# Optimization experiments

Measured on AMD Instinct MI355X. Metric: run time of the kernel, lower is better.

Reference implementation:

```python
import jax, jax.numpy as jnp
import numpy as np

C = 768       # hidden_dim
HEADS = 12    # num_heads
HDIM = C // HEADS  # 64


def _ln(x, w, eps=1e-5):
    # LayerNorm with weight, no bias (matches nn.LayerNorm(..., bias=False))
    mu = jnp.mean(x, axis=-1, keepdims=True)
    var = jnp.mean((x - mu) ** 2, axis=-1, keepdims=True)
    return (x - mu) * jax.lax.rsqrt(var + eps) * w


def _attn(q, k, v):
    # scaled dot product attention over the second-to-last axis
    scale = 1.0 / np.sqrt(q.shape[-1]).astype(np.float32)
    s = jnp.einsum('...qc,...kc->...qk', q, k) * scale
    return jnp.einsum('...qk,...kc->...qc', jax.nn.softmax(s, axis=-1), v)


def setup_inputs() -> dict:
    key = jax.random.key(0)
    ks = jax.random.split(key, 4)
    B, H, W = 4, 64, 64
    x = jax.random.normal(ks[0], (B, H, W, C), jnp.float32)
    Wqkv = jax.random.normal(ks[1], (C, 7 * C), jnp.float32) * 0.02
    bqkv = jnp.zeros((7 * C,), jnp.float32)
    Wout = jax.random.normal(ks[2], (C, C), jnp.float32) * 0.02
    bout = jnp.zeros((C,), jnp.float32)
    Wmlp = jax.random.normal(ks[3], (4 * C, C), jnp.float32) * 0.02
    bmlp = jnp.zeros((C,), jnp.float32)
    norm_w = jnp.ones((C,), jnp.float32)
    qnorm_w = jnp.ones((HDIM,), jnp.float32)
    knorm_w = jnp.ones((HDIM,), jnp.float32)
    gamma = jnp.full((C,), 1e-6, jnp.float32)
    return {"x": x, "norm_w": norm_w, "Wqkv": Wqkv, "bqkv": bqkv,
            "qnorm_w": qnorm_w, "knorm_w": knorm_w, "Wout": Wout,
            "bout": bout, "Wmlp": Wmlp, "bmlp": bmlp, "gamma": gamma}


def reference(x, norm_w, Wqkv, bqkv, qnorm_w, knorm_w, Wout, bout, Wmlp, bmlp, gamma):
    B, H, W, _ = x.shape
    xn = _ln(x, norm_w)
    proj = xn @ Wqkv + bqkv                       # (B,H,W,7C)
    q, k, v, ff = jnp.split(proj, [C, 2 * C, 3 * C], axis=-1)
    heads = lambda t: t.reshape(B, H, W, HEADS, HDIM)
    q, k, v = heads(q), heads(k), heads(v)        # (B,H,W,He,c)
    q = _ln(q, qnorm_w)
    k = _ln(k, knorm_w)

    # --- axis 1: 'b h w he c -> b h he w c', attend over w ---
    q, k, v = (t.transpose(0, 1, 3, 2, 4) for t in (q, k, v))  # (B,H,He,W,c)
    ax = _attn(q, k, v)                                         # (B,H,He,W,c)
    # out_permutation 'b w he h c -> b h w (he c)' applied POSITIONALLY ->
    # the first axis contribution lands spatially transposed (requires H==W)
    out = ax.transpose(0, 3, 1, 2, 4).reshape(B, W, H, C)

    # --- axis 2: 'b h he w c -> b w he h c' (positional), attend over h ---
    q, k, v = (t.transpose(0, 3, 2, 1, 4) for t in (q, k, v))  # (B,W,He,H,c)
    ax = _attn(q, k, v)                                         # (B,W,He,H,c)
    out = out + ax.transpose(0, 3, 1, 2, 4).reshape(B, H, W, C)

    y = out @ Wout + bout + (jax.nn.gelu(ff, approximate=False) @ Wmlp + bmlp)
    return x + gamma * y
```

## Files before the change

kernel.cpp:

```cpp
#include <hip/hip_runtime.h>

typedef unsigned short u16;
typedef unsigned int u32;
typedef unsigned char u8;
typedef long i64;
typedef float f4 __attribute__((ext_vector_type(4)));
typedef int i32x8 __attribute__((ext_vector_type(8)));

#define CDIM 768
#define NPROJ 5376
#define KFF 3840
#define NTOK 16384

__device__ __forceinline__ u8 f2fp8(float f) {
#if __has_builtin(__builtin_amdgcn_cvt_pk_fp8_f32)
    return (u8)(__builtin_amdgcn_cvt_pk_fp8_f32(f, f, 0, false) & 0xff);
#else
    u32 u = __float_as_uint(f);
    u32 s = (u >> 24) & 0x80u;
    float a = fabsf(f);
    a = fminf(a, 448.f);
    if (a < 0.015625f) return (u8)(s | (u32)(a * 512.f + 0.5f));
    u32 b = __float_as_uint(a);
    b += 0x0007FFFFu + ((b >> 20) & 1u);
    u32 e = b >> 23, m = (b >> 20) & 7u;
    u32 code = ((e - 120u) << 3) | m;
    if (code > 0x7Eu) code = 0x7Eu;
    return (u8)(s | code);
#endif
}
__device__ __forceinline__ u32 pk4_fp8(float a, float b, float c, float d) {
#if __has_builtin(__builtin_amdgcn_cvt_pk_fp8_f32)
    u32 lo = (u32)__builtin_amdgcn_cvt_pk_fp8_f32(a, b, 0, false);
    return (u32)__builtin_amdgcn_cvt_pk_fp8_f32(c, d, lo, true);
#else
    return (u32)f2fp8(a) | ((u32)f2fp8(b) << 8) | ((u32)f2fp8(c) << 16) | ((u32)f2fp8(d) << 24);
#endif
}
__device__ __forceinline__ float fp8_to_f32(u32 v) {
#if __has_builtin(__builtin_amdgcn_cvt_f32_fp8)
    return __builtin_amdgcn_cvt_f32_fp8((int)v, 0);
#else
    u32 s = v >> 7, e = (v >> 3) & 15u, m = v & 7u;
    float mag = e ? __uint_as_float(((e + 120u) << 23) | (m << 20))
                  : (float)m * 0.001953125f;
    return s ? -mag : mag;
#endif
}

__device__ __forceinline__ float wsum64(float v) {
#pragma unroll
    for (int m = 32; m > 0; m >>= 1) v += __shfl_xor(v, m, 64);
    return v;
}
__device__ __forceinline__ void gl_lds16(const u8* g, u8* l) {
    __builtin_amdgcn_global_load_lds((__attribute__((address_space(1))) u32*)g,
                                     (__attribute__((address_space(3))) u32*)l,
                                     16, 0, 0);
}

__global__ __launch_bounds__(256) void prep_fused(
    const float* __restrict__ Wqkv, u8* __restrict__ WqkvT,
    const float* __restrict__ Wout, const float* __restrict__ Wmlp,
    u8* __restrict__ BT2,
    const float* __restrict__ x, const float* __restrict__ normw,
    u8* __restrict__ xn) {
    __shared__ float t[32][33];
    const int bid = blockIdx.x;
    const int tid = threadIdx.x;
    if (bid < 6912) {
        const float* src; u8* dst; int R, Cc, dstride, doff, bx, by;
        if (bid < 4032) {
            src = Wqkv; dst = WqkvT; R = CDIM; Cc = NPROJ; dstride = CDIM; doff = 0;
            bx = bid % 168; by = bid / 168;
        } else if (bid < 4608) {
            const int b2 = bid - 4032;
            src = Wout; dst = BT2; R = CDIM; Cc = CDIM; dstride = KFF; doff = 0;
            bx = b2 % 24; by = b2 / 24;
        } else {
            const int b2 = bid - 4608;
            src = Wmlp; dst = BT2; R = 3072; Cc = CDIM; dstride = KFF; doff = 768;
            bx = b2 % 24; by = b2 / 24;
        }
        const int c0 = bx * 32, r0 = by * 32;
        const int tx = tid & 31, ty = tid >> 5;
#pragma unroll
        for (int i = 0; i < 32; i += 8) {
            int r = r0 + ty + i, c = c0 + tx;
            if (r < R && c < Cc) t[ty + i][tx] = src[(size_t)r * Cc + c];
        }
        __syncthreads();
#pragma unroll
        for (int i = 0; i < 32; i += 8) {
            int c = c0 + ty + i, r = r0 + tx;
            if (r < R && c < Cc) dst[(size_t)c * dstride + doff + r] = f2fp8(t[tx][ty + i]);
        }
    } else {
        const int row = (bid - 6912) * 4 + (tid >> 6);
        const int lane = tid & 63;
        const f4* xr = (const f4*)(x + (size_t)row * CDIM);
        const f4* wr = (const f4*)normw;
        f4 v[3];
        float s = 0.f, s2 = 0.f;
#pragma unroll
        for (int i = 0; i < 3; ++i) {
            v[i] = xr[lane + 64 * i];
#pragma unroll
            for (int j = 0; j < 4; ++j) { s += v[i][j]; s2 += v[i][j] * v[i][j]; }
        }
        s = wsum64(s); s2 = wsum64(s2);
        float mu = s * (1.f / 768.f);
        float var = s2 * (1.f / 768.f) - mu * mu;
        float rs = rsqrtf(var + 1e-5f);
        u32* xo = (u32*)(xn + (size_t)row * CDIM);
#pragma unroll
        for (int i = 0; i < 3; ++i) {
            f4 wv = wr[lane + 64 * i];
            xo[lane + 64 * i] = pk4_fp8((v[i][0] - mu) * rs * wv[0], (v[i][1] - mu) * rs * wv[1],
                                        (v[i][2] - mu) * rs * wv[2], (v[i][3] - mu) * rs * wv[3]);
        }
    }
}

template <int MODE>
__global__ __launch_bounds__(256) void gemm_bt(
    const u8* __restrict__ A, const u8* __restrict__ B, int M, int N, int K,
    const float* __restrict__ bias0, const float* __restrict__ bias1,
    const float* __restrict__ xres, const float* __restrict__ gamma,
    u8* __restrict__ oqkv, u8* __restrict__ off, float* __restrict__ ofin) {
    __shared__ __align__(16) u8 As[128 * 128];
    __shared__ __align__(16) u8 Bs[128 * 128];
    const int tid = threadIdx.x;
    const int wid = tid >> 6, lane = tid & 63;
    const int wm = wid >> 1, wn = wid & 1;
    const int quad = lane >> 4, l16 = lane & 15;
    const int m0 = blockIdx.y * 128, n0 = blockIdx.x * 128;

    f4 acc[4][4] = {};

    const int rl = lane >> 3;
    const int csw = ((lane & 7) ^ rl) * 16;
    const u8* aptr[4]; const u8* bptr[4];
    u8* alds[4]; u8* blds[4];
#pragma unroll
    for (int jj = 0; jj < 4; ++jj) {
        const int r0 = wid * 32 + jj * 8;
        aptr[jj] = A + (size_t)(m0 + r0 + rl) * K + csw;
        bptr[jj] = B + (size_t)(n0 + r0 + rl) * K + csw;
        alds[jj] = As + r0 * 128;
        blds[jj] = Bs + r0 * 128;
    }
    const int swl = l16 & 7;

    for (int kt = 0; kt < K; kt += 128) {
#pragma unroll
        for (int jj = 0; jj < 4; ++jj) {
            gl_lds16(aptr[jj] + kt, alds[jj]);
            gl_lds16(bptr[jj] + kt, blds[jj]);
        }
        __syncthreads();
        const int c0 = ((2 * quad) ^ swl) * 16;
        const int c1 = ((2 * quad + 1) ^ swl) * 16;
        i32x8 af[4], bfv[4];
#pragma unroll
        for (int mi = 0; mi < 4; ++mi) {
            const u8* base = As + (wm * 64 + mi * 16 + l16) * 128;
            uint4 lo = *(const uint4*)(base + c0);
            uint4 hi = *(const uint4*)(base + c1);
            af[mi][0] = lo.x; af[mi][1] = lo.y; af[mi][2] = lo.z; af[mi][3] = lo.w;
            af[mi][4] = hi.x; af[mi][5] = hi.y; af[mi][6] = hi.z; af[mi][7] = hi.w;
        }
#pragma unroll
        for (int ni = 0; ni < 4; ++ni) {
            const u8* base = Bs + (wn * 64 + ni * 16 + l16) * 128;
            uint4 lo = *(const uint4*)(base + c0);
            uint4 hi = *(const uint4*)(base + c1);
            bfv[ni][0] = lo.x; bfv[ni][1] = lo.y; bfv[ni][2] = lo.z; bfv[ni][3] = lo.w;
            bfv[ni][4] = hi.x; bfv[ni][5] = hi.y; bfv[ni][6] = hi.z; bfv[ni][7] = hi.w;
        }
#pragma unroll
        for (int mi = 0; mi < 4; ++mi)
#pragma unroll
            for (int ni = 0; ni < 4; ++ni)
                acc[mi][ni] = __builtin_amdgcn_mfma_scale_f32_16x16x128_f8f6f4(
                    af[mi], bfv[ni], acc[mi][ni], 0, 0, 0, 127, 0, 127);
        __syncthreads();
    }

#pragma unroll
    for (int mi = 0; mi < 4; ++mi) {
#pragma unroll
        for (int ni = 0; ni < 4; ++ni) {
            const int col = n0 + wn * 64 + ni * 16 + l16;
            const int rowb = m0 + wm * 64 + mi * 16 + quad * 4;
            if (MODE == 0) {
                const float bc = bias0[col];
#pragma unroll
                for (int r = 0; r < 4; ++r) {
                    float vv = acc[mi][ni][r] + bc;
                    const int m = rowb + r;
                    if (col < 2304) {
                        oqkv[(size_t)m * 2304 + col] = f2fp8(vv);
                    } else {
                        float u2 = vv * (-1.5957691216f) - 0.0713548162f * vv * vv * vv;
                        float g = vv / (1.f + __expf(u2));
                        off[(size_t)m * KFF + 768 + (col - 2304)] = f2fp8(g);
                    }
                }
            } else {
                const float bc = bias0[col] + bias1[col];
                const float gm = gamma[col];
#pragma unroll
                for (int r = 0; r < 4; ++r) {
                    const int m = rowb + r;
                    float vv = acc[mi][ni][r] + bc;
                    ofin[(size_t)m * CDIM + col] = xres[(size_t)m * CDIM + col] + gm * vv;
                }
            }
        }
    }
}

__global__ __launch_bounds__(256) void axial_attn_mfma(const u8* __restrict__ qkv,
                                                       const float* __restrict__ qnw,
                                                       const float* __restrict__ knw,
                                                       u8* __restrict__ A2) {
    __shared__ __align__(16) u8 Qs[64 * 72];
    __shared__ __align__(16) u8 Ks[64 * 72];
    __shared__ __align__(16) u8 Vt[64 * 72];
    __shared__ __align__(16) u8 Ps[64 * 72];

    const int bx = blockIdx.x;
    const int he = bx % 12;
    const int j = (bx / 12) & 63;
    const int b = bx / (12 * 64);
    const int tid = threadIdx.x;
    const int w = tid >> 6, lane = tid & 63;
    const int l16 = lane & 15, quad = lane >> 4;
    const int qb = w * 16;

    f4 acc_o[4] = {};

    const int sr = tid >> 2;
    const int sc = (tid & 3) * 16;
    const f4* qwv = (const f4*)(qnw + sc);
    const f4* kwv = (const f4*)(knw + sc);

    for (int phase = 0; phase < 2; ++phase) {
        const size_t tok = (phase == 0) ? (size_t)((b * 64 + j) * 64 + sr)
                                        : (size_t)((b * 64 + sr) * 64 + j);
        const u8* src = qkv + tok * 2304 + he * 64 + sc;
        {
            uint4 qv = *(const uint4*)(src);
            uint4 kv = *(const uint4*)(src + 768);
            const u32* qu = (const u32*)&qv;
            const u32* ku = (const u32*)&kv;
            float qf[16], kf[16];
#pragma unroll
            for (int jj = 0; jj < 4; ++jj)
#pragma unroll
                for (int bb = 0; bb < 4; ++bb) {
                    qf[jj * 4 + bb] = fp8_to_f32((qu[jj] >> (8 * bb)) & 0xffu);
                    kf[jj * 4 + bb] = fp8_to_f32((ku[jj] >> (8 * bb)) & 0xffu);
                }
            float s1q = 0.f, s2q = 0.f, s1k = 0.f, s2k = 0.f;
#pragma unroll
            for (int i = 0; i < 16; ++i) {
                s1q += qf[i]; s2q += qf[i] * qf[i];
                s1k += kf[i]; s2k += kf[i] * kf[i];
            }
            s1q += __shfl_xor(s1q, 1, 64); s1q += __shfl_xor(s1q, 2, 64);
            s2q += __shfl_xor(s2q, 1, 64); s2q += __shfl_xor(s2q, 2, 64);
            s1k += __shfl_xor(s1k, 1, 64); s1k += __shfl_xor(s1k, 2, 64);
            s2k += __shfl_xor(s2k, 1, 64); s2k += __shfl_xor(s2k, 2, 64);
            const float muq = s1q * (1.f / 64.f), muk = s1k * (1.f / 64.f);
            const float rsq = rsqrtf(s2q * (1.f / 64.f) - muq * muq + 1e-5f);
            const float rsk = rsqrtf(s2k * (1.f / 64.f) - muk * muk + 1e-5f);
            uint4 qo, ko;
            u32* qop = (u32*)&qo; u32* kop = (u32*)&ko;
#pragma unroll
            for (int jj = 0; jj < 4; ++jj) {
                const f4 wq = qwv[jj], wk = kwv[jj];
                qop[jj] = pk4_fp8((qf[jj * 4 + 0] - muq) * rsq * wq[0],
                                  (qf[jj * 4 + 1] - muq) * rsq * wq[1],
                                  (qf[jj * 4 + 2] - muq) * rsq * wq[2],
                                  (qf[jj * 4 + 3] - muq) * rsq * wq[3]);
                kop[jj] = pk4_fp8((kf[jj * 4 + 0] - muk) * rsk * wk[0],
                                  (kf[jj * 4 + 1] - muk) * rsk * wk[1],
                                  (kf[jj * 4 + 2] - muk) * rsk * wk[2],
                                  (kf[jj * 4 + 3] - muk) * rsk * wk[3]);
            }
            *(uint4*)(Qs + sr * 72 + sc) = qo;
            *(uint4*)(Ks + sr * 72 + sc) = ko;
        }
        {
            uint4 vv = *(const uint4*)(src + 1536);
            const u8* vb = (const u8*)&vv;
#pragma unroll
            for (int i = 0; i < 16; ++i) Vt[(sc + i) * 72 + sr] = vb[i];
        }
        __syncthreads();

        f4 st[4] = {};
#pragma unroll
        for (int kt = 0; kt < 2; ++kt) {
            const int boff = (kt * 4 + quad) * 8;
            const i64 bq = *(const i64*)(Qs + (qb + l16) * 72 + boff);
#pragma unroll
            for (int mt = 0; mt < 4; ++mt) {
                const i64 ak = *(const i64*)(Ks + (mt * 16 + l16) * 72 + boff);
                st[mt] = __builtin_amdgcn_mfma_f32_16x16x32_fp8_fp8(ak, bq, st[mt], 0, 0, 0);
            }
        }

        float sv[16];
        float mx = -1e30f;
#pragma unroll
        for (int mt = 0; mt < 4; ++mt)
#pragma unroll
            for (int r = 0; r < 4; ++r) {
                const float s = st[mt][r] * 0.125f;
                sv[mt * 4 + r] = s;
                mx = fmaxf(mx, s);
            }
        mx = fmaxf(mx, __shfl_xor(mx, 16, 64));
        mx = fmaxf(mx, __shfl_xor(mx, 32, 64));
        float sm = 0.f;
#pragma unroll
        for (int i = 0; i < 16; ++i) { sv[i] = __expf(sv[i] - mx); sm += sv[i]; }
        sm += __shfl_xor(sm, 16, 64);
        sm += __shfl_xor(sm, 32, 64);
        const float inv = 1.f / sm;

#pragma unroll
        for (int mt = 0; mt < 4; ++mt) {
            const int kbase = mt * 16 + quad * 4;
            *(u32*)(Ps + (qb + l16) * 72 + kbase) =
                pk4_fp8(sv[mt * 4] * inv, sv[mt * 4 + 1] * inv,
                        sv[mt * 4 + 2] * inv, sv[mt * 4 + 3] * inv);
        }
        __syncthreads();

#pragma unroll
        for (int kt = 0; kt < 2; ++kt) {
            const int boff = (kt * 4 + quad) * 8;
            const i64 ap = *(const i64*)(Ps + (qb + l16) * 72 + boff);
#pragma unroll
            for (int nt = 0; nt < 4; ++nt) {
                const i64 bv = *(const i64*)(Vt + (nt * 16 + l16) * 72 + boff);
                acc_o[nt] = __builtin_amdgcn_mfma_f32_16x16x32_fp8_fp8(ap, bv, acc_o[nt], 0, 0, 0);
            }
        }
        __syncthreads();
    }

#pragma unroll
    for (int nt = 0; nt < 4; ++nt)
#pragma unroll
        for (int r = 0; r < 4; ++r) {
            const int q = qb + quad * 4 + r;
            const int c = nt * 16 + l16;
            A2[((size_t)((b * 64 + q) * 64 + j)) * KFF + he * 64 + c] = f2fp8(acc_o[nt][r]);
        }
}

extern "C" void kernel_launch(void* const* d_in, const int* in_sizes, int n_in,
                              void* d_out, int out_size, void* d_ws, size_t ws_size,
                              hipStream_t stream) {
    const float* x = (const float*)d_in[0];
    const float* normw = (const float*)d_in[1];
    const float* Wqkv = (const float*)d_in[2];
    const float* bqkv = (const float*)d_in[3];
    const float* qnw = (const float*)d_in[4];
    const float* knw = (const float*)d_in[5];
    const float* Wout = (const float*)d_in[6];
    const float* bout = (const float*)d_in[7];
    const float* Wmlp = (const float*)d_in[8];
    const float* bmlp = (const float*)d_in[9];
    const float* gamma = (const float*)d_in[10];
    float* out = (float*)d_out;

    char* ws = (char*)d_ws;
    u8* xn = (u8*)ws;    ws += (size_t)NTOK * CDIM;
    u8* WqkvT = (u8*)ws; ws += (size_t)NPROJ * CDIM;
    u8* BT2 = (u8*)ws;   ws += (size_t)CDIM * KFF;
    u8* qkv = (u8*)ws;   ws += (size_t)NTOK * 2304;
    u8* A2 = (u8*)ws;    ws += (size_t)NTOK * KFF;

    prep_fused<<<11008, 256, 0, stream>>>(Wqkv, WqkvT, Wout, Wmlp, BT2, x, normw, xn);
    gemm_bt<0><<<dim3(NPROJ / 128, NTOK / 128), 256, 0, stream>>>(
        xn, WqkvT, NTOK, NPROJ, CDIM, bqkv, nullptr, nullptr, nullptr, qkv, A2, nullptr);
    axial_attn_mfma<<<3072, 256, 0, stream>>>(qkv, qnw, knw, A2);
    gemm_bt<1><<<dim3(CDIM / 128, NTOK / 128), 256, 0, stream>>>(
        A2, BT2, NTOK, CDIM, KFF, bout, bmlp, x, gamma, nullptr, nullptr, out);
}
```

Measured before the change: 367.9 us.

## Fuse per-head q/k LayerNorm into projection GEMM epilogue and remap block order

```diff
diff --git a/kernel.cpp b/kernel.cpp
--- a/kernel.cpp
+++ b/kernel.cpp
@@ -134,7 +134,12 @@
     const int wid = tid >> 6, lane = tid & 63;
     const int wm = wid >> 1, wn = wid & 1;
     const int quad = lane >> 4, l16 = lane & 15;
-    const int m0 = blockIdx.y * 128, n0 = blockIdx.x * 128;
+
+    const int nbx = (int)gridDim.x;
+    const int nwg = (int)(gridDim.x * gridDim.y);
+    int bid = (int)(blockIdx.y * gridDim.x + blockIdx.x);
+    bid = (bid & 7) * (nwg >> 3) + (bid >> 3);
+    const int m0 = (bid / nbx) * 128, n0 = (bid % nbx) * 128;
 
     f4 acc[4][4] = {};
 
@@ -187,34 +192,74 @@
         __syncthreads();
     }
 
+    const int cbase = n0 + wn * 64;
 #pragma unroll
     for (int mi = 0; mi < 4; ++mi) {
-#pragma unroll
-        for (int ni = 0; ni < 4; ++ni) {
-            const int col = n0 + wn * 64 + ni * 16 + l16;
-            const int rowb = m0 + wm * 64 + mi * 16 + quad * 4;
-            if (MODE == 0) {
-                const float bc = bias0[col];
+        const int rowb = m0 + wm * 64 + mi * 16 + quad * 4;
+        if (MODE == 0) {
+            if (cbase < 1536) {
+                const float* hw = (cbase < 768) ? xres : gamma;
+                float hwv[4], bc[4];
+#pragma unroll
+                for (int ni = 0; ni < 4; ++ni) {
+                    hwv[ni] = hw[ni * 16 + l16];
+                    bc[ni] = bias0[cbase + ni * 16 + l16];
+                }
 #pragma unroll
                 for (int r = 0; r < 4; ++r) {
-                    float vv = acc[mi][ni][r] + bc;
-                    const int m = rowb + r;
-                    if (col < 2304) {
-                        oqkv[(size_t)m * 2304 + col] = f2fp8(vv);
-                    } else {
+                    float v[4]; float s1 = 0.f, s2 = 0.f;
+#pragma unroll
+                    for (int ni = 0; ni < 4; ++ni) {
+                        v[ni] = acc[mi][ni][r] + bc[ni];
+                        s1 += v[ni]; s2 += v[ni] * v[ni];
+                    }
+#pragma unroll
+                    for (int mk = 1; mk <= 8; mk <<= 1) {
+                        s1 += __shfl_xor(s1, mk, 64);
+                        s2 += __shfl_xor(s2, mk, 64);
+                    }
+                    const float mu = s1 * (1.f / 64.f);
+                    const float rs = rsqrtf(s2 * (1.f / 64.f) - mu * mu + 1e-5f);
+                    const size_t m = (size_t)(rowb + r);
+#pragma unroll
+                    for (int ni = 0; ni < 4; ++ni)
+                        oqkv[m * 2304 + cbase + ni * 16 + l16] =
+                            f2fp8((v[ni] - mu) * rs * hwv[ni]);
+                }
+            } else if (cbase < 2304) {
+#pragma unroll
+                for (int ni = 0; ni < 4; ++ni) {
+                    const int col = cbase + ni * 16 + l16;
+                    const float bcv = bias0[col];
+#pragma unroll
+                    for (int r = 0; r < 4; ++r)
+                        oqkv[(size_t)(rowb + r) * 2304 + col] = f2fp8(acc[mi][ni][r] + bcv);
+                }
+            } else {
+#pragma unroll
+                for (int ni = 0; ni < 4; ++ni) {
+                    const int col = cbase + ni * 16 + l16;
+                    const float bcv = bias0[col];
+#pragma unroll
+                    for (int r = 0; r < 4; ++r) {
+                        float vv = acc[mi][ni][r] + bcv;
                         float u2 = vv * (-1.5957691216f) - 0.0713548162f * vv * vv * vv;
                         float g = vv / (1.f + __expf(u2));
-                        off[(size_t)m * KFF + 768 + (col - 2304)] = f2fp8(g);
+                        off[(size_t)(rowb + r) * KFF + 768 + (col - 2304)] = f2fp8(g);
                     }
                 }
-            } else {
-                const float bc = bias0[col] + bias1[col];
+            }
+        } else {
+#pragma unroll
+            for (int ni = 0; ni < 4; ++ni) {
+                const int col = cbase + ni * 16 + l16;
+                const float bcv = bias0[col] + bias1[col];
                 const float gm = gamma[col];
 #pragma unroll
                 for (int r = 0; r < 4; ++r) {
-                    const int m = rowb + r;
-                    float vv = acc[mi][ni][r] + bc;
-                    ofin[(size_t)m * CDIM + col] = xres[(size_t)m * CDIM + col] + gm * vv;
+                    const size_t m = (size_t)(rowb + r);
+                    float vv = acc[mi][ni][r] + bcv;
+                    ofin[m * CDIM + col] = xres[m * CDIM + col] + gm * vv;
                 }
             }
         }
@@ -222,15 +267,14 @@
 }
 
 __global__ __launch_bounds__(256) void axial_attn_mfma(const u8* __restrict__ qkv,
-                                                       const float* __restrict__ qnw,
-                                                       const float* __restrict__ knw,
                                                        u8* __restrict__ A2) {
     __shared__ __align__(16) u8 Qs[64 * 72];
     __shared__ __align__(16) u8 Ks[64 * 72];
     __shared__ __align__(16) u8 Vt[64 * 72];
     __shared__ __align__(16) u8 Ps[64 * 72];
 
-    const int bx = blockIdx.x;
+    int bx = (int)blockIdx.x;
+    bx = (bx & 7) * 384 + (bx >> 3);
     const int he = bx % 12;
     const int j = (bx / 12) & 63;
     const int b = bx / (12 * 64);
@@ -243,8 +287,6 @@
 
     const int sr = tid >> 2;
     const int sc = (tid & 3) * 16;
-    const f4* qwv = (const f4*)(qnw + sc);
-    const f4* kwv = (const f4*)(knw + sc);
 
     for (int phase = 0; phase < 2; ++phase) {
         const size_t tok = (phase == 0) ? (size_t)((b * 64 + j) * 64 + sr)
@@ -253,45 +295,8 @@
         {
             uint4 qv = *(const uint4*)(src);
             uint4 kv = *(const uint4*)(src + 768);
-            const u32* qu = (const u32*)&qv;
-            const u32* ku = (const u32*)&kv;
-            float qf[16], kf[16];
-#pragma unroll
-            for (int jj = 0; jj < 4; ++jj)
-#pragma unroll
-                for (int bb = 0; bb < 4; ++bb) {
-                    qf[jj * 4 + bb] = fp8_to_f32((qu[jj] >> (8 * bb)) & 0xffu);
-                    kf[jj * 4 + bb] = fp8_to_f32((ku[jj] >> (8 * bb)) & 0xffu);
-                }
-            float s1q = 0.f, s2q = 0.f, s1k = 0.f, s2k = 0.f;
-#pragma unroll
-            for (int i = 0; i < 16; ++i) {
-                s1q += qf[i]; s2q += qf[i] * qf[i];
-                s1k += kf[i]; s2k += kf[i] * kf[i];
-            }
-            s1q += __shfl_xor(s1q, 1, 64); s1q += __shfl_xor(s1q, 2, 64);
-            s2q += __shfl_xor(s2q, 1, 64); s2q += __shfl_xor(s2q, 2, 64);
-            s1k += __shfl_xor(s1k, 1, 64); s1k += __shfl_xor(s1k, 2, 64);
-            s2k += __shfl_xor(s2k, 1, 64); s2k += __shfl_xor(s2k, 2, 64);
-            const float muq = s1q * (1.f / 64.f), muk = s1k * (1.f / 64.f);
-            const float rsq = rsqrtf(s2q * (1.f / 64.f) - muq * muq + 1e-5f);
-            const float rsk = rsqrtf(s2k * (1.f / 64.f) - muk * muk + 1e-5f);
-            uint4 qo, ko;
-            u32* qop = (u32*)&qo; u32* kop = (u32*)&ko;
-#pragma unroll
-            for (int jj = 0; jj < 4; ++jj) {
-                const f4 wq = qwv[jj], wk = kwv[jj];
-                qop[jj] = pk4_fp8((qf[jj * 4 + 0] - muq) * rsq * wq[0],
-                                  (qf[jj * 4 + 1] - muq) * rsq * wq[1],
-                                  (qf[jj * 4 + 2] - muq) * rsq * wq[2],
-                                  (qf[jj * 4 + 3] - muq) * rsq * wq[3]);
-                kop[jj] = pk4_fp8((kf[jj * 4 + 0] - muk) * rsk * wk[0],
-                                  (kf[jj * 4 + 1] - muk) * rsk * wk[1],
-                                  (kf[jj * 4 + 2] - muk) * rsk * wk[2],
-                                  (kf[jj * 4 + 3] - muk) * rsk * wk[3]);
-            }
-            *(uint4*)(Qs + sr * 72 + sc) = qo;
-            *(uint4*)(Ks + sr * 72 + sc) = ko;
+            *(uint4*)(Qs + sr * 72 + sc) = qv;
+            *(uint4*)(Ks + sr * 72 + sc) = kv;
         }
         {
             uint4 vv = *(const uint4*)(src + 1536);
@@ -389,8 +394,8 @@
 
     prep_fused<<<11008, 256, 0, stream>>>(Wqkv, WqkvT, Wout, Wmlp, BT2, x, normw, xn);
     gemm_bt<0><<<dim3(NPROJ / 128, NTOK / 128), 256, 0, stream>>>(
-        xn, WqkvT, NTOK, NPROJ, CDIM, bqkv, nullptr, nullptr, nullptr, qkv, A2, nullptr);
-    axial_attn_mfma<<<3072, 256, 0, stream>>>(qkv, qnw, knw, A2);
+        xn, WqkvT, NTOK, NPROJ, CDIM, bqkv, nullptr, qnw, knw, qkv, A2, nullptr);
+    axial_attn_mfma<<<3072, 256, 0, stream>>>(qkv, A2);
     gemm_bt<1><<<dim3(CDIM / 128, NTOK / 128), 256, 0, stream>>>(
         A2, BT2, NTOK, CDIM, KFF, bout, bmlp, x, gamma, nullptr, nullptr, out);
 }
```

Measured after the change: 348.9 us. 5.2% less time.
